# Kernel tuning notes

Hardware: AMD Instinct MI355X
Metric: run time of the kernel (lower is better)

The kernel has to match this reference:

```python
import jax, jax.numpy as jnp
import numpy as np

EPS = 1e-5

def _layernorm(x, w, b):
    mu = jnp.mean(x, axis=-1, keepdims=True)
    var = jnp.var(x, axis=-1, keepdims=True)
    return (x - mu) * jax.lax.rsqrt(var + EPS) * w + b

def setup_inputs() -> dict:
    key = jax.random.key(0)
    ks = jax.random.split(key, 7)
    b, n, m, d, h = 4, 1024, 1024, 1024, 16
    sc = 1.0 / np.sqrt(d)
    return {
        "x": jax.random.normal(ks[0], (b, n, d), jnp.float32),
        "xa": jax.random.normal(ks[1], (b, m, d), jnp.float32),
        "ln_w": jnp.ones((d,), jnp.float32),
        "ln_b": jnp.zeros((d,), jnp.float32),
        "Wq": jax.random.normal(ks[2], (d, d), jnp.float32) * sc,
        "Wkv": jax.random.normal(ks[3], (d, 2 * d), jnp.float32) * sc,
        "Wout": jax.random.normal(ks[4], (d, d), jnp.float32) * sc,
    }

def reference(x, xa, ln_w, ln_b, Wq, Wkv, Wout):
    b, n, d = x.shape
    m = xa.shape[1]
    h = 16
    hd = d // h

    xn = _layernorm(x, ln_w, ln_b)
    xan = _layernorm(xa, ln_w, ln_b)

    q = xn @ Wq                      # [b,n,d]
    kv = xn @ Wkv                    # [b,n,2d] (k,v unused for x->xa path except v)
    k, v = kv[..., :d], kv[..., d:]
    kva = xan @ Wkv
    ka, va = kva[..., :d], kva[..., d:]

    split = lambda t: t.reshape(t.shape[0], t.shape[1], h, hd).transpose(0, 2, 1, 3)  # [b,h,s,hd]
    q, v, ka, va = map(split, (q, v, ka, va))

    # shared score matrix: scores[b,h,n,m] = q . ka  (no scaling in source)
    scores = jnp.einsum('bhnd,bhmd->bhnm', q, ka)
    # x -> attends over xa: softmax over m
    probs_x = jax.nn.softmax(scores, axis=-1)
    x_upd = jnp.einsum('bhnm,bhmd->bhnd', probs_x, va)
    # xa -> attends over x: softmax over n (of transposed scores)
    probs_xa = jax.nn.softmax(scores.transpose(0, 1, 3, 2), axis=-1)  # [b,h,m,n]
    xa_upd = jnp.einsum('bhmn,bhnd->bhmd', probs_xa, v)

    merge = lambda t: t.transpose(0, 2, 1, 3).reshape(t.shape[0], t.shape[2], d)
    return (merge(x_upd) @ Wout, merge(xa_upd) @ Wout)
```

## Files before the change

kernel.cpp:

```cpp
#include <hip/hip_runtime.h>
#include <hip/hip_bf16.h>

typedef unsigned short u16;
typedef unsigned int u32;
typedef __attribute__((ext_vector_type(4))) unsigned short u16x4;
typedef __attribute__((ext_vector_type(8))) unsigned short u16x8;
typedef __attribute__((ext_vector_type(8))) __bf16 bf16x8;
typedef __attribute__((ext_vector_type(4))) float f32x4;

__device__ __forceinline__ u16 f2bf(float f){
  unsigned u = __builtin_bit_cast(unsigned, f);
  u += 0x7FFFu + ((u >> 16) & 1u);
  return (u16)(u >> 16);
}

__device__ __forceinline__ u32 cvtpk(float lo, float hi){
  u32 r;
  asm("v_cvt_pk_bf16_f32 %0, %1, %2" : "=v"(r) : "v"(lo), "v"(hi));
  return r;
}

__device__ __forceinline__ void load_lds16(const void* g, void* l){
  __builtin_amdgcn_global_load_lds((const __attribute__((address_space(1))) unsigned*)g,
                                   (__attribute__((address_space(3))) unsigned*)l, 16, 0, 0);
}

__device__ __forceinline__ void storeC(float* p, float v){ *p = v; }
__device__ __forceinline__ void storeC(u16* p, float v){ *p = f2bf(v); }

__global__ __launch_bounds__(256) void transpose_all(const float* __restrict__ Wq,
                                                     const float* __restrict__ Wkv,
                                                     const float* __restrict__ Wout,
                                                     u16* __restrict__ WqT, u16* __restrict__ WkT,
                                                     u16* __restrict__ WvT, u16* __restrict__ WoT){
  const float* in; u16* out; int ldin;
  switch (blockIdx.z){
    case 0:  in = Wq;         out = WqT; ldin = 1024; break;
    case 1:  in = Wkv;        out = WkT; ldin = 2048; break;
    case 2:  in = Wkv + 1024; out = WvT; ldin = 2048; break;
    default: in = Wout;       out = WoT; ldin = 1024; break;
  }
  float scl = (blockIdx.z == 0) ? 1.44269504f : 1.0f;
  __shared__ float tile[64][65];
  int t = threadIdx.x;
  int tr = blockIdx.y * 64, tc = blockIdx.x * 64;
  int r0 = t >> 4, c0 = (t & 15) * 4;
#pragma unroll
  for (int i = 0; i < 4; ++i){
    int r = r0 + i * 16;
    const float4 val = *(const float4*)&in[(size_t)(tr + r) * ldin + tc + c0];
    tile[r][c0] = val.x; tile[r][c0+1] = val.y; tile[r][c0+2] = val.z; tile[r][c0+3] = val.w;
  }
  __syncthreads();
#pragma unroll
  for (int i = 0; i < 4; ++i){
    int n = r0 + i * 16;
    u16x4 o4;
    o4.x = f2bf(tile[c0+0][n] * scl); o4.y = f2bf(tile[c0+1][n] * scl);
    o4.z = f2bf(tile[c0+2][n] * scl); o4.w = f2bf(tile[c0+3][n] * scl);
    *(u16x4*)&out[(size_t)(tc + n) * 1024 + tr + c0] = o4;
  }
}

__global__ __launch_bounds__(256) void ln_cast(const float* __restrict__ x, const float* __restrict__ xa,
                                               const float* __restrict__ w, const float* __restrict__ bb,
                                               u16* __restrict__ xn, u16* __restrict__ xan){
  int row = blockIdx.x;
  const float* src; u16* dst;
  if (row < 4096){ src = x + (size_t)row * 1024; dst = xn + (size_t)row * 1024; }
  else { src = xa + (size_t)(row - 4096) * 1024; dst = xan + (size_t)(row - 4096) * 1024; }
  int t = threadIdx.x;
  float4 v = ((const float4*)src)[t];
  float s = v.x + v.y + v.z + v.w;
  float ss = v.x*v.x + v.y*v.y + v.z*v.z + v.w*v.w;
#pragma unroll
  for (int o = 32; o > 0; o >>= 1){ s += __shfl_down(s, o); ss += __shfl_down(ss, o); }
  __shared__ float red[8];
  int wv = t >> 6;
  if ((t & 63) == 0){ red[wv] = s; red[wv + 4] = ss; }
  __syncthreads();
  if (t == 0){
    red[0] = red[0] + red[1] + red[2] + red[3];
    red[4] = red[4] + red[5] + red[6] + red[7];
  }
  __syncthreads();
  float mu = red[0] * (1.0f/1024.0f);
  float var = red[4] * (1.0f/1024.0f) - mu*mu;
  float rstd = rsqrtf(var + 1e-5f);
  float4 wv4 = ((const float4*)w)[t];
  float4 bv4 = ((const float4*)bb)[t];
  u16x4 o4;
  o4.x = f2bf((v.x - mu) * rstd * wv4.x + bv4.x);
  o4.y = f2bf((v.y - mu) * rstd * wv4.y + bv4.y);
  o4.z = f2bf((v.z - mu) * rstd * wv4.z + bv4.z);
  o4.w = f2bf((v.w - mu) * rstd * wv4.w + bv4.w);
  ((u16x4*)dst)[t] = o4;
}

template<int BM, int TMASK, typename OutT>
__global__ __launch_bounds__(512, 2) void gemm256(
    const u16* __restrict__ A0, const u16* __restrict__ A1,
    const u16* __restrict__ A2, const u16* __restrict__ A3,
    const u16* __restrict__ B0, const u16* __restrict__ B1,
    const u16* __restrict__ B2, const u16* __restrict__ B3,
    OutT* __restrict__ C0, OutT* __restrict__ C1,
    OutT* __restrict__ C2, OutT* __restrict__ C3){
  constexpr int AI = BM / 64;
  constexpr int FI = BM / 32;
  __shared__ u16 SA[2][BM * 64];
  __shared__ u16 SB[2][16384];
  int tid = threadIdx.x, lane = tid & 63, wave = tid >> 6;
  int g = lane >> 4, r15 = lane & 15;
  int quad = blockIdx.x >> 2, ntile = blockIdx.x & 3;
  int mbase = blockIdx.y * BM, nbase = ntile * 256;
  const u16* A = quad==0?A0:quad==1?A1:quad==2?A2:A3;
  const u16* B = quad==0?B0:quad==1?B1:quad==2?B2:B3;
  OutT* C      = quad==0?C0:quad==1?C1:quad==2?C2:C3;
  int wr = wave >> 2, wc = wave & 3;
  int rsub = lane >> 3;
  int slo  = (lane & 7) ^ ((lane >> 3) & 7);
  int sw8  = (r15 & 7) << 3;
  f32x4 acc[FI][4] = {};

#define STG(kt, b) { \
  int ko = (kt) * 64; \
  _Pragma("unroll") \
  for (int i = 0; i < AI; ++i){ \
    int row = i*64 + wave*8 + rsub; \
    load_lds16(A + (size_t)(mbase + row)*1024 + ko + slo*8, &SA[b][(i*512 + wave*64)*8]); \
  } \
  _Pragma("unroll") \
  for (int i = 0; i < 4; ++i){ \
    int row = i*64 + wave*8 + rsub; \
    load_lds16(B + (size_t)(nbase + row)*1024 + ko + slo*8, &SB[b][(i*512 + wave*64)*8]); \
  } }

  STG(0, 0);
  for (int t = 0; t < 16; ++t){
    int b = t & 1;
    if (t < 15){
      STG(t + 1, b ^ 1);
      if constexpr (AI == 4) asm volatile("s_waitcnt vmcnt(8)" ::: "memory");
      else                   asm volatile("s_waitcnt vmcnt(6)" ::: "memory");
    } else {
      asm volatile("s_waitcnt vmcnt(0)" ::: "memory");
    }
    __builtin_amdgcn_s_barrier();
    __builtin_amdgcn_sched_barrier(0);
    const u16* Al = &SA[b][0];
    const u16* Bl = &SB[b][0];
#pragma unroll
    for (int ks = 0; ks < 2; ++ks){
      bf16x8 af[FI], bfr[4];
#pragma unroll
      for (int fi = 0; fi < FI; ++fi)
        af[fi] = *(const bf16x8*)&Al[(wr*(FI*16) + fi*16 + r15)*64 + ((ks*32 + g*8) ^ sw8)];
#pragma unroll
      for (int fj = 0; fj < 4; ++fj)
        bfr[fj] = *(const bf16x8*)&Bl[(wc*64 + fj*16 + r15)*64 + ((ks*32 + g*8) ^ sw8)];
#pragma unroll
      for (int fi = 0; fi < FI; ++fi)
#pragma unroll
        for (int fj = 0; fj < 4; ++fj)
          acc[fi][fj] = __builtin_amdgcn_mfma_f32_16x16x32_bf16(af[fi], bfr[fj], acc[fi][fj], 0, 0, 0);
    }
    __builtin_amdgcn_s_barrier();
  }
#undef STG

  bool tr = (TMASK >> quad) & 1;
#pragma unroll
  for (int fi = 0; fi < FI; ++fi)
#pragma unroll
    for (int fj = 0; fj < 4; ++fj)
#pragma unroll
      for (int r = 0; r < 4; ++r){
        int row = mbase + wr*(FI*16) + fi*16 + g*4 + r;
        int col = nbase + wc*64 + fj*16 + r15;
        if constexpr (TMASK != 0){
          if (tr){
            int bb = row >> 10, token = row & 1023;
            int hh = col >> 6,  dd = col & 63;
            storeC(&C[((size_t)((bb << 4) + hh) * 64 + dd) * 1024 + token], acc[fi][fj][r]);
            continue;
          }
        }
        storeC(&C[(size_t)row * 1024 + col], acc[fi][fj][r]);
      }
}

#define SW(row, col) ((row) * 64 + ((col) ^ (((row) & 7) << 3)))

__device__ __forceinline__ void exchP(const f32x4& s0, const f32x4& s1,
                                      const f32x4& s2, const f32x4& s3,
                                      bool gh, bool g0, bf16x8& pf0, bf16x8& pf1){
  u32 pk00 = cvtpk(s0[0], s0[1]), pk01 = cvtpk(s0[2], s0[3]);
  u32 pk10 = cvtpk(s1[0], s1[1]), pk11 = cvtpk(s1[2], s1[3]);
  u32 pk20 = cvtpk(s2[0], s2[1]), pk21 = cvtpk(s2[2], s2[3]);
  u32 pk30 = cvtpk(s3[0], s3[1]), pk31 = cvtpk(s3[2], s3[3]);
  u32 c0 = gh ? pk10 : pk00, c1 = gh ? pk11 : pk01;
  u32 d0 = gh ? pk00 : pk10, d1 = gh ? pk01 : pk11;
  u32 s1a = __shfl_xor((int)c0, 16), s1b = __shfl_xor((int)c1, 16);
  u32 s2a = __shfl_xor((int)d0, 32), s2b = __shfl_xor((int)d1, 32);
  u32 s3a = __shfl_xor((int)d0, 48), s3b = __shfl_xor((int)d1, 48);
  union UB { u32 w[4]; bf16x8 v; } ub0, ub1;
  ub0.w[0] = gh ? (g0 ? s1a : s2a) : (g0 ? s3a : c0);
  ub0.w[1] = gh ? (g0 ? s1b : s2b) : (g0 ? s3b : c1);
  ub0.w[2] = gh ? (g0 ? c0 : s3a) : (g0 ? s2a : s1a);
  ub0.w[3] = gh ? (g0 ? c1 : s3b) : (g0 ? s2b : s1b);
  u32 e0 = gh ? pk30 : pk20, e1 = gh ? pk31 : pk21;
  u32 f0 = gh ? pk20 : pk30, f1 = gh ? pk21 : pk31;
  u32 t1a = __shfl_xor((int)e0, 16), t1b = __shfl_xor((int)e1, 16);
  u32 t2a = __shfl_xor((int)f0, 32), t2b = __shfl_xor((int)f1, 32);
  u32 t3a = __shfl_xor((int)f0, 48), t3b = __shfl_xor((int)f1, 48);
  ub1.w[0] = gh ? (g0 ? t1a : t2a) : (g0 ? t3a : e0);
  ub1.w[1] = gh ? (g0 ? t1b : t2b) : (g0 ? t3b : e1);
  ub1.w[2] = gh ? (g0 ? e0 : t3a) : (g0 ? t2a : t1a);
  ub1.w[3] = gh ? (g0 ? e1 : t3b) : (g0 ? t2b : t1b);
  pf0 = ub0.v; pf1 = ub1.v;
}

#define MFMA16(a, b, c) __builtin_amdgcn_mfma_f32_16x16x32_bf16(a, b, c, 0, 0, 0)

__global__ __launch_bounds__(256) void flash(const u16* __restrict__ qg, const u16* __restrict__ vTg,
                                             const u16* __restrict__ kag, const u16* __restrict__ vaTg,
                                             u16* __restrict__ xu, u16* __restrict__ xau){
  __shared__ u16 Ks[4096], VTs[4096];
  int tid = threadIdx.x, lane = tid & 63, wave = tid >> 6, g = lane >> 4, r15 = lane & 15;
  int qt = blockIdx.x, bh = blockIdx.y, dir = blockIdx.z;
  size_t tokbase = ((size_t)(bh >> 4)) * 1048576 + (size_t)(bh & 15) * 64;
  size_t vtbase  = (size_t)bh << 16;
  const u16 *Q, *K, *VT; u16* O;
  if (dir == 0){ Q = qg + tokbase;  K = kag + tokbase; VT = vaTg + vtbase; O = xu  + tokbase; }
  else         { Q = kag + tokbase; K = qg  + tokbase; VT = vTg  + vtbase; O = xau + tokbase; }
  Q += (size_t)qt * 64 * 1024;
  O += (size_t)qt * 64 * 1024;

  int wq = wave * 16;
  bf16x8 qf0 = *(const bf16x8*)&Q[(size_t)(wq + r15) * 1024 + g*8];
  bf16x8 qf1 = *(const bf16x8*)&Q[(size_t)(wq + r15) * 1024 + 32 + g*8];

  int srow = tid >> 3, scol = (tid & 7) * 8;
  const u16* Kp  = K  + (size_t)srow * 1024 + scol;
  const u16* VTp = VT + (size_t)srow * 1024 + scol;
  u16x8 kr0 = *(const u16x8*)(Kp);
  u16x8 kr1 = *(const u16x8*)(Kp + (size_t)32 * 1024);
  u16x8 vr0 = *(const u16x8*)(VTp);
  u16x8 vr1 = *(const u16x8*)(VTp + (size_t)32 * 1024);

  float l = 0.0f;
  f32x4 acc[4] = {};
  bool gh = g >= 2, g0 = g & 1;
  const f32x4 zinit = {-32.f, -32.f, -32.f, -32.f};

  for (int j = 0; j < 16; ++j){
    __syncthreads();
    *(u16x8*)&Ks [SW(srow,      scol)] = kr0;
    *(u16x8*)&Ks [SW(srow + 32, scol)] = kr1;
    *(u16x8*)&VTs[SW(srow,      scol)] = vr0;
    *(u16x8*)&VTs[SW(srow + 32, scol)] = vr1;
    if (j < 15){
      const u16* Kn = Kp  + (size_t)(j + 1) * 64 * 1024;
      const u16* Vn = VTp + (j + 1) * 64;
      kr0 = *(const u16x8*)(Kn);
      kr1 = *(const u16x8*)(Kn + (size_t)32 * 1024);
      vr0 = *(const u16x8*)(Vn);
      vr1 = *(const u16x8*)(Vn + (size_t)32 * 1024);
    }
    __syncthreads();

    f32x4 sf[4];
    __builtin_amdgcn_s_setprio(1);
#pragma unroll
    for (int kvi = 0; kvi < 4; ++kvi){
      bf16x8 kf0 = *(const bf16x8*)&Ks[SW(kvi*16 + r15, g*8)];
      bf16x8 kf1 = *(const bf16x8*)&Ks[SW(kvi*16 + r15, 32 + g*8)];
      f32x4 z = MFMA16(kf0, qf0, zinit);
      z = MFMA16(kf1, qf1, z);
      sf[kvi] = z;
    }
    __builtin_amdgcn_s_setprio(0);

    float psum = 0.0f;
#pragma unroll
    for (int kvi = 0; kvi < 4; ++kvi)
#pragma unroll
      for (int r = 0; r < 4; ++r){
        float p = __builtin_amdgcn_exp2f(sf[kvi][r]);
        sf[kvi][r] = p; psum += p;
      }
    psum += __shfl_xor(psum, 16);
    psum += __shfl_xor(psum, 32);
    l += psum;

    bf16x8 pf0, pf1;
    exchP(sf[0], sf[1], sf[2], sf[3], gh, g0, pf0, pf1);

    __builtin_amdgcn_s_setprio(1);
#pragma unroll
    for (int nb = 0; nb < 4; ++nb){
      bf16x8 vf0 = *(const bf16x8*)&VTs[SW(nb*16 + r15, g*8)];
      acc[nb] = MFMA16(vf0, pf0, acc[nb]);
    }
#pragma unroll
    for (int nb = 0; nb < 4; ++nb){
      bf16x8 vf1 = *(const bf16x8*)&VTs[SW(nb*16 + r15, 32 + g*8)];
      acc[nb] = MFMA16(vf1, pf1, acc[nb]);
    }
    __builtin_amdgcn_s_setprio(0);
  }

  float inv = 1.0f / l;
  size_t orow = (size_t)(wq + r15) * 1024;
#pragma unroll
  for (int nb = 0; nb < 4; ++nb){
    u16x4 o;
    o.x = f2bf(acc[nb][0] * inv);
    o.y = f2bf(acc[nb][1] * inv);
    o.z = f2bf(acc[nb][2] * inv);
    o.w = f2bf(acc[nb][3] * inv);
    *(u16x4*)&O[orow + nb*16 + g*4] = o;
  }
}

extern "C" void kernel_launch(void* const* d_in, const int* in_sizes, int n_in,
                              void* d_out, int out_size, void* d_ws, size_t ws_size,
                              hipStream_t stream){
  const float* x    = (const float*)d_in[0];
  const float* xa   = (const float*)d_in[1];
  const float* lnw  = (const float*)d_in[2];
  const float* lnb  = (const float*)d_in[3];
  const float* Wq   = (const float*)d_in[4];
  const float* Wkv  = (const float*)d_in[5];
  const float* Wout = (const float*)d_in[6];
  float* out = (float*)d_out;
  char* ws = (char*)d_ws;
  const size_t MB = 1ull << 20;
  u16* xn  = (u16*)(ws);
  u16* xan = (u16*)(ws + 8*MB);
  u16* q   = (u16*)(ws + 16*MB);
  u16* vT  = (u16*)(ws + 24*MB);
  u16* ka  = (u16*)(ws + 32*MB);
  u16* vaT = (u16*)(ws + 40*MB);
  u16* xu  = (u16*)(ws + 48*MB);
  u16* xau = (u16*)(ws + 56*MB);
  u16* WqT = (u16*)(ws + 64*MB);
  u16* WkT = (u16*)(ws + 66*MB);
  u16* WvT = (u16*)(ws + 68*MB);
  u16* WoT = (u16*)(ws + 70*MB);
  dim3 blk(256);
  transpose_all<<<dim3(16,16,4), blk, 0, stream>>>(Wq, Wkv, Wout, WqT, WkT, WvT, WoT);
  ln_cast<<<8192, blk, 0, stream>>>(x, xa, lnw, lnb, xn, xan);
  gemm256<256, 0xA, u16><<<dim3(16,16), dim3(512), 0, stream>>>(
      xn, xn, xan, xan, WqT, WvT, WkT, WvT, q, vT, ka, vaT);
  flash<<<dim3(16,64,2), blk, 0, stream>>>(q, vT, ka, vaT, xu, xau);
  gemm256<128, 0, float><<<dim3(4,64), dim3(512), 0, stream>>>(
      xu, xu, xu, xu, WoT, WoT, WoT, WoT, out, out, out, out);
}
```

Before: 172.1 us.

## Shrink GEMM tiles to 128x128 and remap flash blocks for XCD locality

Replaces the 256-wide, 512-thread GEMM with a 128x128-tile, 256-thread kernel, quadrupling the block count for the projection GEMMs so more CUs stay busy. The flash attention launch becomes a 1D grid whose block index is decoded so that all query tiles of one (batch, head, direction) pair land on the same XCD, aiming to improve L2 reuse of K/V. Smaller tiles lower arithmetic intensity per block and raise global traffic. The 8-XCD round-robin assumption is hard-coded.

```diff
diff --git a/kernel.cpp b/kernel.cpp
--- a/kernel.cpp
+++ b/kernel.cpp
@@ -97,42 +97,35 @@
   ((u16x4*)dst)[t] = o4;
 }
 
-template<int BM, int TMASK, typename OutT>
-__global__ __launch_bounds__(512, 2) void gemm256(
+template<int TMASK, typename OutT>
+__global__ __launch_bounds__(256, 2) void gemm128(
     const u16* __restrict__ A0, const u16* __restrict__ A1,
     const u16* __restrict__ A2, const u16* __restrict__ A3,
     const u16* __restrict__ B0, const u16* __restrict__ B1,
     const u16* __restrict__ B2, const u16* __restrict__ B3,
     OutT* __restrict__ C0, OutT* __restrict__ C1,
     OutT* __restrict__ C2, OutT* __restrict__ C3){
-  constexpr int AI = BM / 64;
-  constexpr int FI = BM / 32;
-  __shared__ u16 SA[2][BM * 64];
-  __shared__ u16 SB[2][16384];
+  __shared__ u16 SA[2][8192], SB[2][8192];
   int tid = threadIdx.x, lane = tid & 63, wave = tid >> 6;
   int g = lane >> 4, r15 = lane & 15;
-  int quad = blockIdx.x >> 2, ntile = blockIdx.x & 3;
-  int mbase = blockIdx.y * BM, nbase = ntile * 256;
+  int quad = blockIdx.x >> 3, ntile = blockIdx.x & 7;
+  int mbase = blockIdx.y * 128, nbase = ntile * 128;
   const u16* A = quad==0?A0:quad==1?A1:quad==2?A2:A3;
   const u16* B = quad==0?B0:quad==1?B1:quad==2?B2:B3;
   OutT* C      = quad==0?C0:quad==1?C1:quad==2?C2:C3;
-  int wr = wave >> 2, wc = wave & 3;
+  int wr = wave >> 1, wc = wave & 1;
   int rsub = lane >> 3;
   int slo  = (lane & 7) ^ ((lane >> 3) & 7);
   int sw8  = (r15 & 7) << 3;
-  f32x4 acc[FI][4] = {};
+  f32x4 acc[4][4] = {};
 
 #define STG(kt, b) { \
   int ko = (kt) * 64; \
   _Pragma("unroll") \
-  for (int i = 0; i < AI; ++i){ \
-    int row = i*64 + wave*8 + rsub; \
-    load_lds16(A + (size_t)(mbase + row)*1024 + ko + slo*8, &SA[b][(i*512 + wave*64)*8]); \
-  } \
-  _Pragma("unroll") \
   for (int i = 0; i < 4; ++i){ \
-    int row = i*64 + wave*8 + rsub; \
-    load_lds16(B + (size_t)(nbase + row)*1024 + ko + slo*8, &SB[b][(i*512 + wave*64)*8]); \
+    int row = i*32 + wave*8 + rsub; \
+    load_lds16(A + (size_t)(mbase + row)*1024 + ko + slo*8, &SA[b][(i*256 + wave*64)*8]); \
+    load_lds16(B + (size_t)(nbase + row)*1024 + ko + slo*8, &SB[b][(i*256 + wave*64)*8]); \
   } }
 
   STG(0, 0);
@@ -140,8 +133,7 @@
     int b = t & 1;
     if (t < 15){
       STG(t + 1, b ^ 1);
-      if constexpr (AI == 4) asm volatile("s_waitcnt vmcnt(8)" ::: "memory");
-      else                   asm volatile("s_waitcnt vmcnt(6)" ::: "memory");
+      asm volatile("s_waitcnt vmcnt(8)" ::: "memory");
     } else {
       asm volatile("s_waitcnt vmcnt(0)" ::: "memory");
     }
@@ -151,15 +143,15 @@
     const u16* Bl = &SB[b][0];
 #pragma unroll
     for (int ks = 0; ks < 2; ++ks){
-      bf16x8 af[FI], bfr[4];
-#pragma unroll
-      for (int fi = 0; fi < FI; ++fi)
-        af[fi] = *(const bf16x8*)&Al[(wr*(FI*16) + fi*16 + r15)*64 + ((ks*32 + g*8) ^ sw8)];
+      bf16x8 af[4], bfr[4];
+#pragma unroll
+      for (int fi = 0; fi < 4; ++fi)
+        af[fi] = *(const bf16x8*)&Al[(wr*64 + fi*16 + r15)*64 + ((ks*32 + g*8) ^ sw8)];
 #pragma unroll
       for (int fj = 0; fj < 4; ++fj)
         bfr[fj] = *(const bf16x8*)&Bl[(wc*64 + fj*16 + r15)*64 + ((ks*32 + g*8) ^ sw8)];
 #pragma unroll
-      for (int fi = 0; fi < FI; ++fi)
+      for (int fi = 0; fi < 4; ++fi)
 #pragma unroll
         for (int fj = 0; fj < 4; ++fj)
           acc[fi][fj] = __builtin_amdgcn_mfma_f32_16x16x32_bf16(af[fi], bfr[fj], acc[fi][fj], 0, 0, 0);
@@ -170,12 +162,12 @@
 
   bool tr = (TMASK >> quad) & 1;
 #pragma unroll
-  for (int fi = 0; fi < FI; ++fi)
+  for (int fi = 0; fi < 4; ++fi)
 #pragma unroll
     for (int fj = 0; fj < 4; ++fj)
 #pragma unroll
       for (int r = 0; r < 4; ++r){
-        int row = mbase + wr*(FI*16) + fi*16 + g*4 + r;
+        int row = mbase + wr*64 + fi*16 + g*4 + r;
         int col = nbase + wc*64 + fj*16 + r15;
         if constexpr (TMASK != 0){
           if (tr){
@@ -227,7 +219,11 @@
                                              u16* __restrict__ xu, u16* __restrict__ xau){
   __shared__ u16 Ks[4096], VTs[4096];
   int tid = threadIdx.x, lane = tid & 63, wave = tid >> 6, g = lane >> 4, r15 = lane & 15;
-  int qt = blockIdx.x, bh = blockIdx.y, dir = blockIdx.z;
+  int b = blockIdx.x;
+  int xcd = b & 7, idx = b >> 3;
+  int qt = idx & 15;
+  int pair = xcd * 16 + (idx >> 4);
+  int bh = pair & 63, dir = pair >> 6;
   size_t tokbase = ((size_t)(bh >> 4)) * 1048576 + (size_t)(bh & 15) * 64;
   size_t vtbase  = (size_t)bh << 16;
   const u16 *Q, *K, *VT; u16* O;
@@ -351,9 +347,9 @@
   dim3 blk(256);
   transpose_all<<<dim3(16,16,4), blk, 0, stream>>>(Wq, Wkv, Wout, WqT, WkT, WvT, WoT);
   ln_cast<<<8192, blk, 0, stream>>>(x, xa, lnw, lnb, xn, xan);
-  gemm256<256, 0xA, u16><<<dim3(16,16), dim3(512), 0, stream>>>(
+  gemm128<0xA, u16><<<dim3(32,32), blk, 0, stream>>>(
       xn, xn, xan, xan, WqT, WvT, WkT, WvT, q, vT, ka, vaT);
-  flash<<<dim3(16,64,2), blk, 0, stream>>>(q, vT, ka, vaT, xu, xau);
-  gemm256<128, 0, float><<<dim3(4,64), dim3(512), 0, stream>>>(
+  flash<<<dim3(2048), blk, 0, stream>>>(q, vT, ka, vaT, xu, xau);
+  gemm128<0, float><<<dim3(8,64), blk, 0, stream>>>(
       xu, xu, xu, xu, WoT, WoT, WoT, WoT, out, out, out, out);
 }
```

Measured after the change: 168.8 us. About the same (-1.9%).
